# Optimization experiments

Measured on AMD Instinct MI355X. Metric: run time of the kernel, lower is better.

Reference implementation:

```python
import jax, jax.numpy as jnp
import numpy as np

B, IDF, RES = 32, 64, 128
CDF, SRC_L, A_DIM = 768, 18, 100
QUERY_L = RES * RES


def setup_inputs() -> dict:
    key = jax.random.key(0)
    ks = jax.random.split(key, 5)
    inputs = jax.random.normal(ks[0], (B, IDF, RES, RES), dtype=jnp.float32)
    context = jax.random.normal(ks[1], (B, CDF, SRC_L), dtype=jnp.float32)
    conv_ctx_w = jax.random.normal(ks[2], (IDF, CDF), dtype=jnp.float32) * (1.0 / np.sqrt(CDF))
    conv_w = jax.random.normal(ks[3], (IDF,), dtype=jnp.float32) * (1.0 / np.sqrt(IDF))
    conv_b = jnp.zeros((1,), dtype=jnp.float32)
    fc_w = jax.random.normal(ks[4], (A_DIM, QUERY_L), dtype=jnp.float32) * (1.0 / np.sqrt(QUERY_L))
    fc_b = jnp.zeros((A_DIM,), dtype=jnp.float32)
    return {"inputs": inputs, "context": context, "conv_ctx_w": conv_ctx_w,
            "conv_w": conv_w, "conv_b": conv_b, "fc_w": fc_w, "fc_b": fc_b}


def reference(inputs, context, conv_ctx_w, conv_w, conv_b, fc_w, fc_b):
    b, idf, ih, iw = inputs.shape
    queryL = ih * iw
    # target: [b, idf, queryL]
    target = inputs.reshape(b, idf, queryL)
    # 1x1 conv on context (conv_context): [b, idf, sourceL]
    sourceT = jnp.einsum('ic,bcs->bis', conv_ctx_w, context)
    # attn scores: [b, queryL, sourceL]; softmax over sourceL (dim=1 on flattened view)
    attn = jnp.einsum('biq,bis->bqs', target, sourceT)
    attn = jax.nn.softmax(attn, axis=-1)
    # weighted context: [b, idf, queryL]
    wctx = jnp.einsum('bis,bqs->biq', sourceT, attn)
    # 1x1 conv to single channel (self.conv): [b, queryL]
    wctx = jnp.einsum('i,biq->bq', conv_w, wctx) + conv_b
    # att_fc: [b, a_dim]
    out = wctx @ fc_w.T + fc_b
    return out
```

## Files before the change

### kernel.cpp

```cpp
#include <hip/hip_runtime.h>

#define BB 32
#define IDF 64
#define QL 16384
#define CDF 768
#define SL 18
#define SLP 20
#define ADIM 100

__device__ __forceinline__ void fma4(float4& a, const float4 v, const float s) {
    a.x += v.x * s; a.y += v.y * s; a.z += v.z * s; a.w += v.w * s;
}

__global__ __launch_bounds__(256, 2) void k1_source(
        const float* __restrict__ ctx,
        const float* __restrict__ wic,
        float* __restrict__ sT)
{
    __shared__ __align__(16) float ctx_l[CDF * SLP];
    const int b = blockIdx.x;
    const int g = blockIdx.y;
    const float* ctxb = ctx + (size_t)b * CDF * SL;

    for (int t = threadIdx.x; t < CDF * SL; t += 256) {
        const int c = t / SL;
        const int s = t - c * SL;
        ctx_l[c * SLP + s] = ctxb[t];
    }
    __syncthreads();

    const int wave = threadIdx.x >> 6;
    const int lane = threadIdx.x & 63;
    const int i0 = g * 16 + wave * 4;

    float acc[4][SL];
#pragma unroll
    for (int ii = 0; ii < 4; ii++)
#pragma unroll
        for (int s = 0; s < SL; s++) acc[ii][s] = 0.f;

    for (int k = 0; k < CDF / 64; k++) {
        const int c = k * 64 + lane;
        float wv[4];
#pragma unroll
        for (int ii = 0; ii < 4; ii++) wv[ii] = wic[(i0 + ii) * CDF + c];
        float r[SLP];
        const float4* r4 = (const float4*)&ctx_l[c * SLP];
        ((float4*)r)[0] = r4[0];
        ((float4*)r)[1] = r4[1];
        ((float4*)r)[2] = r4[2];
        ((float4*)r)[3] = r4[3];
        ((float4*)r)[4] = r4[4];
#pragma unroll
        for (int ii = 0; ii < 4; ii++)
#pragma unroll
            for (int s = 0; s < SL; s++) acc[ii][s] += wv[ii] * r[s];
    }

#pragma unroll
    for (int ii = 0; ii < 4; ii++) {
#pragma unroll
        for (int s = 0; s < SL; s++) {
            float a = acc[ii][s];
#pragma unroll
            for (int off = 32; off; off >>= 1) a += __shfl_xor(a, off, 64);
            if (lane == 0) sT[((size_t)b * IDF + i0 + ii) * SLP + s] = a;
        }
    }
}

__global__ __launch_bounds__(256, 2) void k2_attn(
        const float* __restrict__ inp,
        const float* __restrict__ sT,
        const float* __restrict__ conv_w,
        const float* __restrict__ conv_b,
        float* __restrict__ wq)
{
    __shared__ __align__(16) float st_l[IDF * SLP];
    __shared__ float cw_l[IDF];
    __shared__ float v_l[SL];
    const int b = blockIdx.y;
    const int tid = threadIdx.x;

    for (int t = tid; t < IDF * SLP; t += 256) st_l[t] = sT[(size_t)b * IDF * SLP + t];
    if (tid < IDF) cw_l[tid] = conv_w[tid];
    __syncthreads();
    if (tid < SL) {
        float a = 0.f;
#pragma unroll
        for (int i = 0; i < IDF; i++) a += cw_l[i] * st_l[i * SLP + tid];
        v_l[tid] = a;
    }
    __syncthreads();

    const int q = (blockIdx.x * 256 + tid) * 4;
    const float4* ip4 = (const float4*)(inp + (size_t)b * IDF * QL + q);

    float4 sc[SL];
#pragma unroll
    for (int s = 0; s < SL; s++) sc[s] = make_float4(0.f, 0.f, 0.f, 0.f);

#pragma unroll 8
    for (int i = 0; i < IDF; i++) {
        const float4 x = ip4[i * (QL / 4)];
        float r[SLP];
        const float4* r4 = (const float4*)&st_l[i * SLP];
        ((float4*)r)[0] = r4[0];
        ((float4*)r)[1] = r4[1];
        ((float4*)r)[2] = r4[2];
        ((float4*)r)[3] = r4[3];
        ((float4*)r)[4] = r4[4];
#pragma unroll
        for (int s = 0; s < SL; s++) fma4(sc[s], x, r[s]);
    }

    float4 m = sc[0];
#pragma unroll
    for (int s = 1; s < SL; s++) {
        m.x = fmaxf(m.x, sc[s].x); m.y = fmaxf(m.y, sc[s].y);
        m.z = fmaxf(m.z, sc[s].z); m.w = fmaxf(m.w, sc[s].w);
    }
    float4 l = make_float4(0.f, 0.f, 0.f, 0.f);
    float4 o = make_float4(0.f, 0.f, 0.f, 0.f);
#pragma unroll
    for (int s = 0; s < SL; s++) {
        const float vs = v_l[s];
        float4 p;
        p.x = __expf(sc[s].x - m.x); p.y = __expf(sc[s].y - m.y);
        p.z = __expf(sc[s].z - m.z); p.w = __expf(sc[s].w - m.w);
        l.x += p.x; l.y += p.y; l.z += p.z; l.w += p.w;
        o.x += p.x * vs; o.y += p.y * vs; o.z += p.z * vs; o.w += p.w * vs;
    }
    const float cb = conv_b[0];
    float4 res;
    res.x = o.x / l.x + cb; res.y = o.y / l.y + cb;
    res.z = o.z / l.z + cb; res.w = o.w / l.w + cb;
    ((float4*)(wq + (size_t)b * QL))[blockIdx.x * 256 + tid] = res;
}

__global__ __launch_bounds__(256, 2) void k3_fc(
        const float* __restrict__ wq,
        const float* __restrict__ fcw,
        const float* __restrict__ fc_b,
        float* __restrict__ out)
{
    __shared__ float part[4 * 16];
    const int b4 = blockIdx.x / 25;
    const int ag = blockIdx.x - b4 * 25;
    const int b0 = b4 * 4, a0 = ag * 4;
    const int wave = threadIdx.x >> 6;
    const int lane = threadIdx.x & 63;
    const int q0 = wave * 4096;

    float4 acc[4][4];
#pragma unroll
    for (int i = 0; i < 4; i++)
#pragma unroll
        for (int j = 0; j < 4; j++) acc[i][j] = make_float4(0.f, 0.f, 0.f, 0.f);

#pragma unroll 2
    for (int k = 0; k < 16; k++) {
        const int qi = q0 + (k * 64 + lane) * 4;
        float4 wv[4], fv[4];
#pragma unroll
        for (int i = 0; i < 4; i++) wv[i] = *(const float4*)(wq + (size_t)(b0 + i) * QL + qi);
#pragma unroll
        for (int j = 0; j < 4; j++) fv[j] = *(const float4*)(fcw + (size_t)(a0 + j) * QL + qi);
#pragma unroll
        for (int i = 0; i < 4; i++) {
#pragma unroll
            for (int j = 0; j < 4; j++) {
                acc[i][j].x += wv[i].x * fv[j].x;
                acc[i][j].y += wv[i].y * fv[j].y;
                acc[i][j].z += wv[i].z * fv[j].z;
                acc[i][j].w += wv[i].w * fv[j].w;
            }
        }
    }

#pragma unroll
    for (int i = 0; i < 4; i++) {
#pragma unroll
        for (int j = 0; j < 4; j++) {
            float r = acc[i][j].x + acc[i][j].y + acc[i][j].z + acc[i][j].w;
#pragma unroll
            for (int off = 32; off; off >>= 1) r += __shfl_xor(r, off, 64);
            if (lane == 0) part[wave * 16 + i * 4 + j] = r;
        }
    }
    __syncthreads();
    if (threadIdx.x < 16) {
        const int i = threadIdx.x >> 2;
        const int j = threadIdx.x & 3;
        const float s = part[threadIdx.x] + part[16 + threadIdx.x] +
                        part[32 + threadIdx.x] + part[48 + threadIdx.x];
        out[(b0 + i) * ADIM + a0 + j] = s + fc_b[a0 + j];
    }
}

extern "C" void kernel_launch(void* const* d_in, const int* in_sizes, int n_in,
                              void* d_out, int out_size, void* d_ws, size_t ws_size,
                              hipStream_t stream)
{
    const float* inputs     = (const float*)d_in[0];
    const float* context    = (const float*)d_in[1];
    const float* conv_ctx_w = (const float*)d_in[2];
    const float* conv_w     = (const float*)d_in[3];
    const float* conv_b     = (const float*)d_in[4];
    const float* fc_w       = (const float*)d_in[5];
    const float* fc_b       = (const float*)d_in[6];
    float* out = (float*)d_out;

    float* ws = (float*)d_ws;
    float* sT = ws;
    float* wq = ws + (size_t)BB * IDF * SLP;

    k1_source<<<dim3(BB, 4), dim3(256), 0, stream>>>(context, conv_ctx_w, sT);
    k2_attn<<<dim3(QL / 1024, BB), dim3(256), 0, stream>>>(inputs, sT, conv_w, conv_b, wq);
    k3_fc<<<dim3(200), dim3(256), 0, stream>>>(wq, fc_w, fc_b, out);
}
```

Measured before the change: 273.3 us.

## Prefetch input chunks in attention kernel and split FC reduction with atomics

The attention kernel now loads the 64 input channels in chunks of eight float4s, issuing the loads for the next chunk before computing on the current one (software double buffering) to hide global load latency. The FC kernel splits the query dimension across more waves (400 blocks instead of 200, each wave covering a 2048-wide slice). Partial sums go straight to the output via atomicAdd, and the bias is pre-written to the output by the first kernel. This raises parallelism in the FC stage, at the cost of more registers in the attention kernel and float atomics with nondeterministic summation order.

```diff
diff --git a/kernel.cpp b/kernel.cpp
--- a/kernel.cpp
+++ b/kernel.cpp
@@ -15,13 +15,20 @@
 __global__ __launch_bounds__(256, 2) void k1_source(
         const float* __restrict__ ctx,
         const float* __restrict__ wic,
-        float* __restrict__ sT)
+        const float* __restrict__ fc_b,
+        float* __restrict__ sT,
+        float* __restrict__ out)
 {
     __shared__ __align__(16) float ctx_l[CDF * SLP];
     const int b = blockIdx.x;
     const int g = blockIdx.y;
+
+    if (g == 0) {
+        const int t = b * 256 + threadIdx.x;
+        if (t < BB * ADIM) out[t] = fc_b[t % ADIM];
+    }
+
     const float* ctxb = ctx + (size_t)b * CDF * SL;
-
     for (int t = threadIdx.x; t < CDF * SL; t += 256) {
         const int c = t / SL;
         const int s = t - c * SL;
@@ -100,18 +107,34 @@
 #pragma unroll
     for (int s = 0; s < SL; s++) sc[s] = make_float4(0.f, 0.f, 0.f, 0.f);
 
-#pragma unroll 8
-    for (int i = 0; i < IDF; i++) {
-        const float4 x = ip4[i * (QL / 4)];
-        float r[SLP];
-        const float4* r4 = (const float4*)&st_l[i * SLP];
-        ((float4*)r)[0] = r4[0];
-        ((float4*)r)[1] = r4[1];
-        ((float4*)r)[2] = r4[2];
-        ((float4*)r)[3] = r4[3];
-        ((float4*)r)[4] = r4[4];
-#pragma unroll
-        for (int s = 0; s < SL; s++) fma4(sc[s], x, r[s]);
+    float4 xa[8];
+#pragma unroll
+    for (int j = 0; j < 8; j++) xa[j] = ip4[(size_t)j * (QL / 4)];
+
+#pragma unroll
+    for (int c = 0; c < 8; c++) {
+        float4 xb[8];
+        if (c < 7) {
+#pragma unroll
+            for (int j = 0; j < 8; j++) xb[j] = ip4[(size_t)((c + 1) * 8 + j) * (QL / 4)];
+        }
+#pragma unroll
+        for (int j = 0; j < 8; j++) {
+            const int i = c * 8 + j;
+            float r[SLP];
+            const float4* r4 = (const float4*)&st_l[i * SLP];
+            ((float4*)r)[0] = r4[0];
+            ((float4*)r)[1] = r4[1];
+            ((float4*)r)[2] = r4[2];
+            ((float4*)r)[3] = r4[3];
+            ((float4*)r)[4] = r4[4];
+#pragma unroll
+            for (int s = 0; s < SL; s++) fma4(sc[s], xa[j], r[s]);
+        }
+        if (c < 7) {
+#pragma unroll
+            for (int j = 0; j < 8; j++) xa[j] = xb[j];
+        }
     }
 
     float4 m = sc[0];
@@ -141,16 +164,15 @@
 __global__ __launch_bounds__(256, 2) void k3_fc(
         const float* __restrict__ wq,
         const float* __restrict__ fcw,
-        const float* __restrict__ fc_b,
         float* __restrict__ out)
 {
-    __shared__ float part[4 * 16];
-    const int b4 = blockIdx.x / 25;
-    const int ag = blockIdx.x - b4 * 25;
-    const int b0 = b4 * 4, a0 = ag * 4;
-    const int wave = threadIdx.x >> 6;
+    const int w = blockIdx.x * 4 + (threadIdx.x >> 6);
     const int lane = threadIdx.x & 63;
-    const int q0 = wave * 4096;
+    const int b4 = w / 200;
+    const int rem = w - b4 * 200;
+    const int ag = rem >> 3;
+    const int qc = rem & 7;
+    const int b0 = b4 * 4, a0 = ag * 4, q0 = qc * 2048;
 
     float4 acc[4][4];
 #pragma unroll
@@ -158,8 +180,8 @@
 #pragma unroll
         for (int j = 0; j < 4; j++) acc[i][j] = make_float4(0.f, 0.f, 0.f, 0.f);
 
-#pragma unroll 2
-    for (int k = 0; k < 16; k++) {
+#pragma unroll 4
+    for (int k = 0; k < 8; k++) {
         const int qi = q0 + (k * 64 + lane) * 4;
         float4 wv[4], fv[4];
 #pragma unroll
@@ -185,16 +207,8 @@
             float r = acc[i][j].x + acc[i][j].y + acc[i][j].z + acc[i][j].w;
 #pragma unroll
             for (int off = 32; off; off >>= 1) r += __shfl_xor(r, off, 64);
-            if (lane == 0) part[wave * 16 + i * 4 + j] = r;
-        }
-    }
-    __syncthreads();
-    if (threadIdx.x < 16) {
-        const int i = threadIdx.x >> 2;
-        const int j = threadIdx.x & 3;
-        const float s = part[threadIdx.x] + part[16 + threadIdx.x] +
-                        part[32 + threadIdx.x] + part[48 + threadIdx.x];
-        out[(b0 + i) * ADIM + a0 + j] = s + fc_b[a0 + j];
+            if (lane == 0) atomicAdd(&out[(b0 + i) * ADIM + a0 + j], r);
+        }
     }
 }
 
@@ -215,7 +229,7 @@
     float* sT = ws;
     float* wq = ws + (size_t)BB * IDF * SLP;
 
-    k1_source<<<dim3(BB, 4), dim3(256), 0, stream>>>(context, conv_ctx_w, sT);
+    k1_source<<<dim3(BB, 4), dim3(256), 0, stream>>>(context, conv_ctx_w, fc_b, sT, out);
     k2_attn<<<dim3(QL / 1024, BB), dim3(256), 0, stream>>>(inputs, sT, conv_w, conv_b, wq);
-    k3_fc<<<dim3(200), dim3(256), 0, stream>>>(wq, fc_w, fc_b, out);
-}
+    k3_fc<<<dim3(400), dim3(256), 0, stream>>>(wq, fc_w, out);
+}
```

Result: no change. 271.7 us (-0.6%).

## Fuse attention and FC projection into one kernel with atomic accumulation

Applied to the files above, without the earlier changes.

The final FC matvec moves into the attention kernel. Each block keeps its 1024-query slice of the conv output in shared memory, takes dot products against the matching fc_w slice for all 100 outputs, and accumulates into the output with atomicAdd. The bias is written ahead of time by the source kernel. This removes the intermediate wq write and read and one kernel launch, at the cost of rereading fc_w once per batch (32x through L2) and 51200 atomic adds, with a summation order that is no longer deterministic.

```diff
diff --git a/kernel.cpp b/kernel.cpp
--- a/kernel.cpp
+++ b/kernel.cpp
@@ -12,16 +12,23 @@
     a.x += v.x * s; a.y += v.y * s; a.z += v.z * s; a.w += v.w * s;
 }
 
-__global__ __launch_bounds__(256, 2) void k1_source(
+__global__ __launch_bounds__(256, 2) void kA_source(
         const float* __restrict__ ctx,
         const float* __restrict__ wic,
-        float* __restrict__ sT)
+        const float* __restrict__ fc_b,
+        float* __restrict__ sT,
+        float* __restrict__ out)
 {
     __shared__ __align__(16) float ctx_l[CDF * SLP];
     const int b = blockIdx.x;
     const int g = blockIdx.y;
+
+    if (g == 0) {
+        const int t = b * 256 + threadIdx.x;
+        if (t < BB * ADIM) out[t] = fc_b[t % ADIM];
+    }
+
     const float* ctxb = ctx + (size_t)b * CDF * SL;
-
     for (int t = threadIdx.x; t < CDF * SL; t += 256) {
         const int c = t / SL;
         const int s = t - c * SL;
@@ -69,18 +76,23 @@
     }
 }
 
-__global__ __launch_bounds__(256, 2) void k2_attn(
+__global__ __launch_bounds__(256, 2) void kB_attn_fc(
         const float* __restrict__ inp,
         const float* __restrict__ sT,
         const float* __restrict__ conv_w,
         const float* __restrict__ conv_b,
-        float* __restrict__ wq)
+        const float* __restrict__ fcw,
+        float* __restrict__ out)
 {
     __shared__ __align__(16) float st_l[IDF * SLP];
+    __shared__ __align__(16) float wq_l[1024];
     __shared__ float cw_l[IDF];
     __shared__ float v_l[SL];
-    const int b = blockIdx.y;
+    const int b  = blockIdx.y;
+    const int qt = blockIdx.x;
     const int tid = threadIdx.x;
+    const int wave = tid >> 6;
+    const int lane = tid & 63;
 
     for (int t = tid; t < IDF * SLP; t += 256) st_l[t] = sT[(size_t)b * IDF * SLP + t];
     if (tid < IDF) cw_l[tid] = conv_w[tid];
@@ -93,7 +105,7 @@
     }
     __syncthreads();
 
-    const int q = (blockIdx.x * 256 + tid) * 4;
+    const int q = (qt * 256 + tid) * 4;
     const float4* ip4 = (const float4*)(inp + (size_t)b * IDF * QL + q);
 
     float4 sc[SL];
@@ -102,7 +114,7 @@
 
 #pragma unroll 8
     for (int i = 0; i < IDF; i++) {
-        const float4 x = ip4[i * (QL / 4)];
+        const float4 x = ip4[(size_t)i * (QL / 4)];
         float r[SLP];
         const float4* r4 = (const float4*)&st_l[i * SLP];
         ((float4*)r)[0] = r4[0];
@@ -135,66 +147,25 @@
     float4 res;
     res.x = o.x / l.x + cb; res.y = o.y / l.y + cb;
     res.z = o.z / l.z + cb; res.w = o.w / l.w + cb;
-    ((float4*)(wq + (size_t)b * QL))[blockIdx.x * 256 + tid] = res;
-}
+    ((float4*)wq_l)[tid] = res;
+    __syncthreads();
 
-__global__ __launch_bounds__(256, 2) void k3_fc(
-        const float* __restrict__ wq,
-        const float* __restrict__ fcw,
-        const float* __restrict__ fc_b,
-        float* __restrict__ out)
-{
-    __shared__ float part[4 * 16];
-    const int b4 = blockIdx.x / 25;
-    const int ag = blockIdx.x - b4 * 25;
-    const int b0 = b4 * 4, a0 = ag * 4;
-    const int wave = threadIdx.x >> 6;
-    const int lane = threadIdx.x & 63;
-    const int q0 = wave * 4096;
-
-    float4 acc[4][4];
+    const float* fcw_t = fcw + (size_t)qt * 1024;
+#pragma unroll 1
+    for (int aa = 0; aa < 25; aa++) {
+        const int a = wave * 25 + aa;
+        const float* fr = fcw_t + (size_t)a * QL;
+        float acc = 0.f;
 #pragma unroll
-    for (int i = 0; i < 4; i++)
+        for (int pass = 0; pass < 4; pass++) {
+            const int qi = pass * 256 + lane * 4;
+            const float4 f = *(const float4*)(fr + qi);
+            const float4 w = *(const float4*)(wq_l + qi);
+            acc += f.x * w.x + f.y * w.y + f.z * w.z + f.w * w.w;
+        }
 #pragma unroll
-        for (int j = 0; j < 4; j++) acc[i][j] = make_float4(0.f, 0.f, 0.f, 0.f);
-
-#pragma unroll 2
-    for (int k = 0; k < 16; k++) {
-        const int qi = q0 + (k * 64 + lane) * 4;
-        float4 wv[4], fv[4];
-#pragma unroll
-        for (int i = 0; i < 4; i++) wv[i] = *(const float4*)(wq + (size_t)(b0 + i) * QL + qi);
-#pragma unroll
-        for (int j = 0; j < 4; j++) fv[j] = *(const float4*)(fcw + (size_t)(a0 + j) * QL + qi);
-#pragma unroll
-        for (int i = 0; i < 4; i++) {
-#pragma unroll
-            for (int j = 0; j < 4; j++) {
-                acc[i][j].x += wv[i].x * fv[j].x;
-                acc[i][j].y += wv[i].y * fv[j].y;
-                acc[i][j].z += wv[i].z * fv[j].z;
-                acc[i][j].w += wv[i].w * fv[j].w;
-            }
-        }
-    }
-
-#pragma unroll
-    for (int i = 0; i < 4; i++) {
-#pragma unroll
-        for (int j = 0; j < 4; j++) {
-            float r = acc[i][j].x + acc[i][j].y + acc[i][j].z + acc[i][j].w;
-#pragma unroll
-            for (int off = 32; off; off >>= 1) r += __shfl_xor(r, off, 64);
-            if (lane == 0) part[wave * 16 + i * 4 + j] = r;
-        }
-    }
-    __syncthreads();
-    if (threadIdx.x < 16) {
-        const int i = threadIdx.x >> 2;
-        const int j = threadIdx.x & 3;
-        const float s = part[threadIdx.x] + part[16 + threadIdx.x] +
-                        part[32 + threadIdx.x] + part[48 + threadIdx.x];
-        out[(b0 + i) * ADIM + a0 + j] = s + fc_b[a0 + j];
+        for (int off = 32; off; off >>= 1) acc += __shfl_xor(acc, off, 64);
+        if (lane == 0) atomicAdd(&out[b * ADIM + a], acc);
     }
 }
 
@@ -213,9 +184,7 @@
 
     float* ws = (float*)d_ws;
     float* sT = ws;
-    float* wq = ws + (size_t)BB * IDF * SLP;
 
-    k1_source<<<dim3(BB, 4), dim3(256), 0, stream>>>(context, conv_ctx_w, sT);
-    k2_attn<<<dim3(QL / 1024, BB), dim3(256), 0, stream>>>(inputs, sT, conv_w, conv_b, wq);
-    k3_fc<<<dim3(200), dim3(256), 0, stream>>>(wq, fc_w, fc_b, out);
+    kA_source<<<dim3(BB, 4), dim3(256), 0, stream>>>(context, conv_ctx_w, fc_b, sT, out);
+    kB_attn_fc<<<dim3(16, BB), dim3(256), 0, stream>>>(inputs, sT, conv_w, conv_b, fc_w, out);
 }
```

Result: no change. 271.7 us (-0.6%).
